# Optimization experiments

Hardware: AMD Instinct MI355X
Metric: run time of the kernel (lower is better)

## Reference

```python
import jax, jax.numpy as jnp
import numpy as np

NUM_NODES = 50000
EMBED_DIM = 64
NUM_EDGES = 1250000
NUM_LAYERS = 3


def setup_inputs() -> dict:
    key = jax.random.key(0)
    k1, k2 = jax.random.split(key)
    edge_index = jax.random.randint(k1, (2, NUM_EDGES), 0, NUM_NODES, dtype=jnp.int64) \
        if jax.config.read('jax_enable_x64') else \
        jax.random.randint(k1, (2, NUM_EDGES), 0, NUM_NODES, dtype=jnp.int32)
    embedding_weight = jax.random.normal(k2, (NUM_NODES, EMBED_DIM), dtype=jnp.float32)
    return {"edge_index": edge_index, "embedding_weight": embedding_weight}


def reference(edge_index, embedding_weight):
    row, col = edge_index[0], edge_index[1]
    n = embedding_weight.shape[0]
    # degree via bincount(row): count of outgoing entries per row index
    deg = jax.ops.segment_sum(
        jnp.ones_like(row, dtype=embedding_weight.dtype), row, num_segments=n)
    # deg^{-1/2} with 0-degree nodes -> 0 (torch sets inf -> 0)
    deg_inv_sqrt = jnp.where(deg > 0, jax.lax.rsqrt(jnp.maximum(deg, 1.0)) * jnp.where(deg > 0, 1.0, 0.0) + jax.lax.rsqrt(jnp.maximum(deg, 1.0)) * 0.0, 0.0)
    deg_inv_sqrt = jnp.where(deg > 0, jax.lax.rsqrt(jnp.maximum(deg, 1.0)), 0.0)
    x = embedding_weight
    acc = x  # running sum of layer embeddings (layer 0 included)
    for _ in range(NUM_LAYERS):
        # gather + degree-norm scale: m[e] = d^{-1/2}[row[e]] * x[col[e]]
        m = deg_inv_sqrt[row][:, None] * x[col]  # [E, D]
        # scatter-add over rows, then right-normalize
        x = jax.ops.segment_sum(m, row, num_segments=n) * deg_inv_sqrt[:, None]
        acc = acc + x
    return acc / (NUM_LAYERS + 1)
```

## Files before the change

kernel.cpp:

```cpp
#include <hip/hip_runtime.h>
#include <hip/hip_fp8.h>

#define NN 50000
#define DIM 64
#define NE 1250000
#define NPARTS 196

#define NSL 64
#define SLICEB 19532
#define RANGE 6250
#define CSTRIDE 50048

typedef __attribute__((ext_vector_type(2))) float f32x2;

__device__ __forceinline__ unsigned short f2b(float f) {
    unsigned int b = __builtin_bit_cast(unsigned int, f);
    b = (b + 0x7fffu + ((b >> 16) & 1u)) >> 16;
    return (unsigned short)b;
}
__device__ __forceinline__ float blo(unsigned int u) {
    return __builtin_bit_cast(float, u << 16);
}
__device__ __forceinline__ float bhi(unsigned int u) {
    return __builtin_bit_cast(float, u & 0xffff0000u);
}

template <bool HI>
__device__ __forceinline__ f32x2 dec2(unsigned int u) {
#if __has_builtin(__builtin_amdgcn_cvt_pk_f32_fp8)
    return __builtin_amdgcn_cvt_pk_f32_fp8(u, HI);
#else
    unsigned int b0 = HI ? ((u >> 16) & 0xff) : (u & 0xff);
    unsigned int b1 = HI ? ((u >> 24) & 0xff) : ((u >> 8) & 0xff);
    __hip_fp8_e4m3 t0, t1;
    t0.__x = (unsigned char)b0;
    t1.__x = (unsigned char)b1;
    f32x2 r;
    r[0] = (float)t0;
    r[1] = (float)t1;
    return r;
#endif
}
__device__ __forceinline__ unsigned int enc4(float v0, float v1, float v2, float v3) {
#if __has_builtin(__builtin_amdgcn_cvt_pk_fp8_f32)
    unsigned int r = 0;
    r = __builtin_amdgcn_cvt_pk_fp8_f32(v0, v1, r, false);
    r = __builtin_amdgcn_cvt_pk_fp8_f32(v2, v3, r, true);
    return r;
#else
    __hip_fp8_e4m3 t0(v0), t1(v1), t2(v2), t3(v3);
    return (unsigned int)t0.__x | ((unsigned int)t1.__x << 8) |
           ((unsigned int)t2.__x << 16) | ((unsigned int)t3.__x << 24);
#endif
}

__global__ __launch_bounds__(256) void k_cvt(const float* __restrict__ in,
                                             unsigned char* __restrict__ out8) {
    int t = blockIdx.x * blockDim.x + threadIdx.x;
    if (t >= NN * DIM / 8) return;
    const float4* p = (const float4*)in + t * 2;
    float4 a = p[0], b = p[1];
    uint2 pk;
    pk.x = enc4(a.x, a.y, a.z, a.w);
    pk.y = enc4(b.x, b.y, b.z, b.w);
    ((uint2*)out8)[t] = pk;
}

__global__ __launch_bounds__(1024) void k_hist(const int* __restrict__ row,
                                               unsigned short* __restrict__ cnt) {
    __shared__ int h[RANGE];
    int bid = blockIdx.x;
    int s   = (bid & 7) | ((bid >> 6) << 3);
    int rng = (bid >> 3) & 7;
    int lo = rng * RANGE;
    int tid = threadIdx.x;
    for (int i = tid; i < RANGE; i += 1024) h[i] = 0;
    __syncthreads();
    int beg = s * SLICEB;
    int end = beg + SLICEB;
    if (end > NE) end = NE;
    for (int e = beg + tid; e < end; e += 1024) {
        int r = row[e] - lo;
        if ((unsigned)r < RANGE) atomicAdd(&h[r], 1);
    }
    __syncthreads();
    unsigned short* c = cnt + s * CSTRIDE + lo;
    for (int i = tid; i < RANGE; i += 1024) c[i] = (unsigned short)h[i];
}

__global__ __launch_bounds__(256) void k_rowscan(unsigned short* __restrict__ cnt,
                                                 int* __restrict__ deg,
                                                 int* __restrict__ partial) {
    __shared__ int sred[256];
    int t = threadIdx.x;
    int r = blockIdx.x * 256 + t;
    int acc = 0;
    if (r < NN) {
#pragma unroll
        for (int s = 0; s < NSL; ++s) {
            int c = cnt[s * CSTRIDE + r];
            cnt[s * CSTRIDE + r] = (unsigned short)acc;
            acc += c;
        }
        deg[r] = acc;
    }
    sred[t] = acc;
    __syncthreads();
    for (int off = 128; off > 0; off >>= 1) {
        if (t < off) sred[t] += sred[t + off];
        __syncthreads();
    }
    if (t == 0) partial[blockIdx.x] = sred[0];
}

__global__ __launch_bounds__(256) void k_scan_top(int* __restrict__ partial) {
    __shared__ int s[256];
    int t = threadIdx.x;
    int v = (t < NPARTS) ? partial[t] : 0;
    s[t] = v;
    __syncthreads();
    for (int off = 1; off < 256; off <<= 1) {
        int x = (t >= off) ? s[t - off] : 0;
        __syncthreads();
        s[t] += x;
        __syncthreads();
    }
    if (t < NPARTS) partial[t] = s[t] - v;
}

__global__ __launch_bounds__(256) void k_scan_final(const int* __restrict__ deg,
                                                    const int* __restrict__ partial,
                                                    int* __restrict__ offs) {
    __shared__ int s[256];
    int t = threadIdx.x;
    int i = blockIdx.x * 256 + t;
    int v = (i < NN) ? deg[i] : 0;
    s[t] = v;
    __syncthreads();
    for (int off = 1; off < 256; off <<= 1) {
        int x = (t >= off) ? s[t - off] : 0;
        __syncthreads();
        s[t] += x;
        __syncthreads();
    }
    int excl = s[t] - v;
    if (i <= NN) offs[i] = partial[blockIdx.x] + excl;
}

__global__ __launch_bounds__(1024) void k_fillb(const int* __restrict__ row,
                                                const int* __restrict__ col,
                                                const int* __restrict__ offs,
                                                const unsigned short* __restrict__ cnt,
                                                int* __restrict__ csr) {
    __shared__ int cur[RANGE];
    int bid = blockIdx.x;
    int s   = bid >> 3;
    int rng = bid & 7;
    int lo = rng * RANGE;
    int tid = threadIdx.x;
    const unsigned short* c = cnt + s * CSTRIDE + lo;
    const int* o = offs + lo;
    for (int i = tid; i < RANGE; i += 1024) cur[i] = o[i] + c[i];
    __syncthreads();
    int beg = s * SLICEB;
    int end = beg + SLICEB;
    if (end > NE) end = NE;
    int e = beg + tid;
    for (; e + 3 * 1024 < end; e += 4 * 1024) {
        int r0 = __builtin_nontemporal_load(&row[e]) - lo;
        int r1 = __builtin_nontemporal_load(&row[e + 1024]) - lo;
        int r2 = __builtin_nontemporal_load(&row[e + 2048]) - lo;
        int r3 = __builtin_nontemporal_load(&row[e + 3072]) - lo;
        if ((unsigned)r0 < RANGE) {
            int pos = atomicAdd(&cur[r0], 1);
            csr[pos] = __builtin_nontemporal_load(&col[e]);
        }
        if ((unsigned)r1 < RANGE) {
            int pos = atomicAdd(&cur[r1], 1);
            csr[pos] = __builtin_nontemporal_load(&col[e + 1024]);
        }
        if ((unsigned)r2 < RANGE) {
            int pos = atomicAdd(&cur[r2], 1);
            csr[pos] = __builtin_nontemporal_load(&col[e + 2048]);
        }
        if ((unsigned)r3 < RANGE) {
            int pos = atomicAdd(&cur[r3], 1);
            csr[pos] = __builtin_nontemporal_load(&col[e + 3072]);
        }
    }
    for (; e < end; e += 1024) {
        int r = __builtin_nontemporal_load(&row[e]) - lo;
        if ((unsigned)r < RANGE) {
            int pos = atomicAdd(&cur[r], 1);
            csr[pos] = __builtin_nontemporal_load(&col[e]);
        }
    }
}

template <int PHASE>
__global__ __launch_bounds__(256) void k_layer(const unsigned char* __restrict__ xin8,
                                               const float* __restrict__ emb,
                                               const unsigned short* __restrict__ xa16,
                                               const unsigned short* __restrict__ xb16,
                                               unsigned short* __restrict__ xout16,
                                               unsigned char* __restrict__ xout8,
                                               float* __restrict__ out,
                                               const int* __restrict__ offs,
                                               const int* __restrict__ csr) {
    int wid = (blockIdx.x * blockDim.x + threadIdx.x) >> 6;
    int lane = threadIdx.x & 63;
    int sub = lane >> 3;
    int sl = lane & 7;
    int n = 8 * wid + sub;
    if (n >= NN) return;
    int beg = offs[n];
    int end = offs[n + 1];
    const unsigned char* xq = xin8 + sl * 8;

    float a0 = 0.f, a1 = 0.f, a2 = 0.f, a3 = 0.f, a4 = 0.f, a5 = 0.f, a6 = 0.f, a7 = 0.f;
    float b0 = 0.f, b1 = 0.f, b2 = 0.f, b3 = 0.f, b4 = 0.f, b5 = 0.f, b6 = 0.f, b7 = 0.f;
    int e = beg;
    for (; e + 8 <= end; e += 8) {
        int c0 = csr[e + 0], c1 = csr[e + 1], c2 = csr[e + 2], c3 = csr[e + 3];
        int c4 = csr[e + 4], c5 = csr[e + 5], c6 = csr[e + 6], c7 = csr[e + 7];
        uint2 u0 = *(const uint2*)(xq + c0 * 64);
        uint2 u1 = *(const uint2*)(xq + c1 * 64);
        uint2 u2 = *(const uint2*)(xq + c2 * 64);
        uint2 u3 = *(const uint2*)(xq + c3 * 64);
        uint2 u4 = *(const uint2*)(xq + c4 * 64);
        uint2 u5 = *(const uint2*)(xq + c5 * 64);
        uint2 u6 = *(const uint2*)(xq + c6 * 64);
        uint2 u7 = *(const uint2*)(xq + c7 * 64);
        f32x2 p;
        p = dec2<false>(u0.x); a0 += p[0]; a1 += p[1];
        p = dec2<true >(u0.x); a2 += p[0]; a3 += p[1];
        p = dec2<false>(u0.y); a4 += p[0]; a5 += p[1];
        p = dec2<true >(u0.y); a6 += p[0]; a7 += p[1];
        p = dec2<false>(u1.x); b0 += p[0]; b1 += p[1];
        p = dec2<true >(u1.x); b2 += p[0]; b3 += p[1];
        p = dec2<false>(u1.y); b4 += p[0]; b5 += p[1];
        p = dec2<true >(u1.y); b6 += p[0]; b7 += p[1];
        p = dec2<false>(u2.x); a0 += p[0]; a1 += p[1];
        p = dec2<true >(u2.x); a2 += p[0]; a3 += p[1];
        p = dec2<false>(u2.y); a4 += p[0]; a5 += p[1];
        p = dec2<true >(u2.y); a6 += p[0]; a7 += p[1];
        p = dec2<false>(u3.x); b0 += p[0]; b1 += p[1];
        p = dec2<true >(u3.x); b2 += p[0]; b3 += p[1];
        p = dec2<false>(u3.y); b4 += p[0]; b5 += p[1];
        p = dec2<true >(u3.y); b6 += p[0]; b7 += p[1];
        p = dec2<false>(u4.x); a0 += p[0]; a1 += p[1];
        p = dec2<true >(u4.x); a2 += p[0]; a3 += p[1];
        p = dec2<false>(u4.y); a4 += p[0]; a5 += p[1];
        p = dec2<true >(u4.y); a6 += p[0]; a7 += p[1];
        p = dec2<false>(u5.x); b0 += p[0]; b1 += p[1];
        p = dec2<true >(u5.x); b2 += p[0]; b3 += p[1];
        p = dec2<false>(u5.y); b4 += p[0]; b5 += p[1];
        p = dec2<true >(u5.y); b6 += p[0]; b7 += p[1];
        p = dec2<false>(u6.x); a0 += p[0]; a1 += p[1];
        p = dec2<true >(u6.x); a2 += p[0]; a3 += p[1];
        p = dec2<false>(u6.y); a4 += p[0]; a5 += p[1];
        p = dec2<true >(u6.y); a6 += p[0]; a7 += p[1];
        p = dec2<false>(u7.x); b0 += p[0]; b1 += p[1];
        p = dec2<true >(u7.x); b2 += p[0]; b3 += p[1];
        p = dec2<false>(u7.y); b4 += p[0]; b5 += p[1];
        p = dec2<true >(u7.y); b6 += p[0]; b7 += p[1];
    }
    for (; e < end; ++e) {
        uint2 u = *(const uint2*)(xq + csr[e] * 64);
        f32x2 p;
        p = dec2<false>(u.x); a0 += p[0]; a1 += p[1];
        p = dec2<true >(u.x); a2 += p[0]; a3 += p[1];
        p = dec2<false>(u.y); a4 += p[0]; a5 += p[1];
        p = dec2<true >(u.y); a6 += p[0]; a7 += p[1];
    }

    int d = end - beg;
    float inv = (d > 0) ? 1.0f / (float)d : 0.0f;
    float v0 = (a0 + b0) * inv;
    float v1 = (a1 + b1) * inv;
    float v2 = (a2 + b2) * inv;
    float v3 = (a3 + b3) * inv;
    float v4 = (a4 + b4) * inv;
    float v5 = (a5 + b5) * inv;
    float v6 = (a6 + b6) * inv;
    float v7 = (a7 + b7) * inv;

    int o = n * DIM + sl * 8;
    if (PHASE < 2) {
        uint4 pk16 = {(unsigned int)f2b(v0) | ((unsigned int)f2b(v1) << 16),
                      (unsigned int)f2b(v2) | ((unsigned int)f2b(v3) << 16),
                      (unsigned int)f2b(v4) | ((unsigned int)f2b(v5) << 16),
                      (unsigned int)f2b(v6) | ((unsigned int)f2b(v7) << 16)};
        *(uint4*)(xout16 + o) = pk16;
        uint2 pk8;
        pk8.x = enc4(v0, v1, v2, v3);
        pk8.y = enc4(v4, v5, v6, v7);
        *(uint2*)(xout8 + o) = pk8;
    } else {
        float4 e0 = *(const float4*)(emb + o);
        float4 e1 = *(const float4*)(emb + o + 4);
        uint4 ua = *(const uint4*)(xa16 + o);
        uint4 ub = *(const uint4*)(xb16 + o);
        float4 o0, o1;
        o0.x = 0.25f * (e0.x + blo(ua.x) + blo(ub.x) + v0);
        o0.y = 0.25f * (e0.y + bhi(ua.x) + bhi(ub.x) + v1);
        o0.z = 0.25f * (e0.z + blo(ua.y) + blo(ub.y) + v2);
        o0.w = 0.25f * (e0.w + bhi(ua.y) + bhi(ub.y) + v3);
        o1.x = 0.25f * (e1.x + blo(ua.z) + blo(ub.z) + v4);
        o1.y = 0.25f * (e1.y + bhi(ua.z) + bhi(ub.z) + v5);
        o1.z = 0.25f * (e1.z + blo(ua.w) + blo(ub.w) + v6);
        o1.w = 0.25f * (e1.w + bhi(ua.w) + bhi(ub.w) + v7);
        *(float4*)(out + o) = o0;
        *(float4*)(out + o + 4) = o1;
    }
}

extern "C" void kernel_launch(void* const* d_in, const int* in_sizes, int n_in,
                              void* d_out, int out_size, void* d_ws, size_t ws_size,
                              hipStream_t stream) {
    const int* edge = (const int*)d_in[0];
    const int* row = edge;
    const int* col = edge + NE;
    const float* emb = (const float*)d_in[1];
    float* out = (float*)d_out;

    int* deg    = (int*)d_ws;
    int* offs   = deg + 50048;
    int* partial= offs + 50112;
    int* csr    = partial + 256;
    unsigned short* cnt = (unsigned short*)(csr + 1250048);
    unsigned short* xa16 = cnt + (size_t)NSL * CSTRIDE;
    unsigned short* xb16 = xa16 + NN * DIM;
    unsigned char* x08 = (unsigned char*)(xb16 + NN * DIM);
    unsigned char* xa8 = x08 + NN * DIM;
    unsigned char* xb8 = xa8 + NN * DIM;

    k_cvt       <<<(NN * DIM / 8 + 255) / 256, 256, 0, stream>>>(emb, x08);
    k_hist      <<<NSL * 8, 1024, 0, stream>>>(row, cnt);
    k_rowscan   <<<NPARTS, 256, 0, stream>>>(cnt, deg, partial);
    k_scan_top  <<<1, 256, 0, stream>>>(partial);
    k_scan_final<<<NPARTS, 256, 0, stream>>>(deg, partial, offs);
    k_fillb     <<<NSL * 8, 1024, 0, stream>>>(row, col, offs, cnt, csr);

    int layer_blocks = 1563;
    k_layer<0><<<layer_blocks, 256, 0, stream>>>(x08, nullptr, nullptr, nullptr, xa16, xa8, nullptr, offs, csr);
    k_layer<1><<<layer_blocks, 256, 0, stream>>>(xa8, nullptr, nullptr, nullptr, xb16, xb8, nullptr, offs, csr);
    k_layer<2><<<layer_blocks, 256, 0, stream>>>(xb8, emb, xa16, xb16, nullptr, nullptr, out, offs, csr);
}
```

Baseline: 117.4 us.

## Compact per-range edges in histogram pass so CSR fill reads only staged entries

The histogram kernel now also writes each in-range edge, packed as (local row << 16 | col), into a per-block staging buffer. It uses a wave ballot plus one shared atomic per wave to reserve slots, and records the per-block count. The CSR fill kernel then walks only those staged entries instead of rescanning the whole row/col slice for each of the 8 row ranges. This removes the repeated row reads in the fill step, at the cost of extra ballot/shuffle work and staging writes in the histogram step. It also needs a large staging region in the workspace and relies on node ids fitting in 16 bits.

```diff
diff --git a/kernel.cpp b/kernel.cpp
--- a/kernel.cpp
+++ b/kernel.cpp
@@ -67,25 +67,43 @@
 }
 
 __global__ __launch_bounds__(1024) void k_hist(const int* __restrict__ row,
-                                               unsigned short* __restrict__ cnt) {
+                                               const int* __restrict__ col,
+                                               unsigned short* __restrict__ cnt,
+                                               unsigned int* __restrict__ stage,
+                                               int* __restrict__ bsize) {
     __shared__ int h[RANGE];
+    __shared__ int bcnt;
     int bid = blockIdx.x;
     int s   = (bid & 7) | ((bid >> 6) << 3);
     int rng = (bid >> 3) & 7;
     int lo = rng * RANGE;
     int tid = threadIdx.x;
     for (int i = tid; i < RANGE; i += 1024) h[i] = 0;
+    if (tid == 0) bcnt = 0;
     __syncthreads();
     int beg = s * SLICEB;
     int end = beg + SLICEB;
     if (end > NE) end = NE;
+    unsigned int* st = stage + (size_t)(s * 8 + rng) * SLICEB;
+    int lane = tid & 63;
     for (int e = beg + tid; e < end; e += 1024) {
         int r = row[e] - lo;
-        if ((unsigned)r < RANGE) atomicAdd(&h[r], 1);
+        bool ok = (unsigned)r < RANGE;
+        unsigned long long mask = __ballot(ok);
+        if (ok) {
+            int leader = __ffsll((long long)mask) - 1;
+            int base = 0;
+            if (lane == leader) base = atomicAdd(&bcnt, __popcll(mask));
+            base = __shfl(base, leader);
+            int off = __popcll(mask & ((1ull << lane) - 1ull));
+            st[base + off] = ((unsigned int)r << 16) | (unsigned int)col[e];
+            atomicAdd(&h[r], 1);
+        }
     }
     __syncthreads();
     unsigned short* c = cnt + s * CSTRIDE + lo;
     for (int i = tid; i < RANGE; i += 1024) c[i] = (unsigned short)h[i];
+    if (tid == 0) bsize[s * 8 + rng] = bcnt;
 }
 
 __global__ __launch_bounds__(256) void k_rowscan(unsigned short* __restrict__ cnt,
@@ -147,8 +165,8 @@
     if (i <= NN) offs[i] = partial[blockIdx.x] + excl;
 }
 
-__global__ __launch_bounds__(1024) void k_fillb(const int* __restrict__ row,
-                                                const int* __restrict__ col,
+__global__ __launch_bounds__(1024) void k_fillb(const unsigned int* __restrict__ stage,
+                                                const int* __restrict__ bsize,
                                                 const int* __restrict__ offs,
                                                 const unsigned short* __restrict__ cnt,
                                                 int* __restrict__ csr) {
@@ -162,38 +180,13 @@
     const int* o = offs + lo;
     for (int i = tid; i < RANGE; i += 1024) cur[i] = o[i] + c[i];
     __syncthreads();
-    int beg = s * SLICEB;
-    int end = beg + SLICEB;
-    if (end > NE) end = NE;
-    int e = beg + tid;
-    for (; e + 3 * 1024 < end; e += 4 * 1024) {
-        int r0 = __builtin_nontemporal_load(&row[e]) - lo;
-        int r1 = __builtin_nontemporal_load(&row[e + 1024]) - lo;
-        int r2 = __builtin_nontemporal_load(&row[e + 2048]) - lo;
-        int r3 = __builtin_nontemporal_load(&row[e + 3072]) - lo;
-        if ((unsigned)r0 < RANGE) {
-            int pos = atomicAdd(&cur[r0], 1);
-            csr[pos] = __builtin_nontemporal_load(&col[e]);
-        }
-        if ((unsigned)r1 < RANGE) {
-            int pos = atomicAdd(&cur[r1], 1);
-            csr[pos] = __builtin_nontemporal_load(&col[e + 1024]);
-        }
-        if ((unsigned)r2 < RANGE) {
-            int pos = atomicAdd(&cur[r2], 1);
-            csr[pos] = __builtin_nontemporal_load(&col[e + 2048]);
-        }
-        if ((unsigned)r3 < RANGE) {
-            int pos = atomicAdd(&cur[r3], 1);
-            csr[pos] = __builtin_nontemporal_load(&col[e + 3072]);
-        }
-    }
-    for (; e < end; e += 1024) {
-        int r = __builtin_nontemporal_load(&row[e]) - lo;
-        if ((unsigned)r < RANGE) {
-            int pos = atomicAdd(&cur[r], 1);
-            csr[pos] = __builtin_nontemporal_load(&col[e]);
-        }
+    int nb = bsize[s * 8 + rng];
+    const unsigned int* st = stage + (size_t)(s * 8 + rng) * SLICEB;
+    for (int i = tid; i < nb; i += 1024) {
+        unsigned int pk = st[i];
+        int r = pk >> 16;
+        int pos = atomicAdd(&cur[r], 1);
+        csr[pos] = (int)(pk & 0xffffu);
     }
 }
 
@@ -327,20 +320,22 @@
     int* deg    = (int*)d_ws;
     int* offs   = deg + 50048;
     int* partial= offs + 50112;
-    int* csr    = partial + 256;
+    int* bsize  = partial + 256;
+    int* csr    = bsize + 576;
     unsigned short* cnt = (unsigned short*)(csr + 1250048);
     unsigned short* xa16 = cnt + (size_t)NSL * CSTRIDE;
     unsigned short* xb16 = xa16 + NN * DIM;
     unsigned char* x08 = (unsigned char*)(xb16 + NN * DIM);
     unsigned char* xa8 = x08 + NN * DIM;
     unsigned char* xb8 = xa8 + NN * DIM;
+    unsigned int* stage = (unsigned int*)(xb8 + NN * DIM);
 
     k_cvt       <<<(NN * DIM / 8 + 255) / 256, 256, 0, stream>>>(emb, x08);
-    k_hist      <<<NSL * 8, 1024, 0, stream>>>(row, cnt);
+    k_hist      <<<NSL * 8, 1024, 0, stream>>>(row, col, cnt, stage, bsize);
     k_rowscan   <<<NPARTS, 256, 0, stream>>>(cnt, deg, partial);
     k_scan_top  <<<1, 256, 0, stream>>>(partial);
     k_scan_final<<<NPARTS, 256, 0, stream>>>(deg, partial, offs);
-    k_fillb     <<<NSL * 8, 1024, 0, stream>>>(row, col, offs, cnt, csr);
+    k_fillb     <<<NSL * 8, 1024, 0, stream>>>(stage, bsize, offs, cnt, csr);
 
     int layer_blocks = 1563;
     k_layer<0><<<layer_blocks, 256, 0, stream>>>(x08, nullptr, nullptr, nullptr, xa16, xa8, nullptr, offs, csr);
```

Result: faster. 102.0 us (-13.1%).
